# Performance work log

Measured on AMD Instinct MI355X. Metric: run time of the kernel, lower is better.

Reference implementation:

```python
import jax, jax.numpy as jnp
import numpy as np

D_MODEL = 41
D_STATE = 16
D_CONV = 4
EXPAND = 2
D_INNER = EXPAND * D_MODEL  # 82
DT_RANK = (D_MODEL + D_STATE - 1) // D_STATE  # ceil(41/16) = 3
NUM_LABELS = 10
B, L = 32, 8192


def setup_inputs() -> dict:
    key = jax.random.key(0)
    ks = jax.random.split(key, 12)
    s = 0.02
    inp = {
        "input": jax.random.normal(ks[0], (B, L, D_MODEL), dtype=jnp.float32),
        # Mamba params
        "in_proj_w": jax.random.normal(ks[1], (2 * D_INNER, D_MODEL), dtype=jnp.float32) * s,
        "conv_w": jax.random.normal(ks[2], (D_INNER, D_CONV), dtype=jnp.float32) * s,
        "conv_b": jnp.zeros((D_INNER,), dtype=jnp.float32),
        "x_proj_w": jax.random.normal(ks[3], (DT_RANK + 2 * D_STATE, D_INNER), dtype=jnp.float32) * s,
        "dt_proj_w": jax.random.normal(ks[4], (D_INNER, DT_RANK), dtype=jnp.float32) * s,
        "dt_proj_b": jax.random.normal(ks[5], (D_INNER,), dtype=jnp.float32) * s,
        "A_log": jnp.log(jnp.broadcast_to(jnp.arange(1, D_STATE + 1, dtype=jnp.float32), (D_INNER, D_STATE))),
        "D": jnp.ones((D_INNER,), dtype=jnp.float32),
        "out_proj_w": jax.random.normal(ks[6], (D_MODEL, D_INNER), dtype=jnp.float32) * s,
        # classifier
        "cls_w": jax.random.normal(ks[7], (NUM_LABELS, D_MODEL), dtype=jnp.float32) * s,
        "cls_b": jnp.zeros((NUM_LABELS,), dtype=jnp.float32),
    }
    return inp


def _mamba(x, in_proj_w, conv_w, conv_b, x_proj_w, dt_proj_w, dt_proj_b, A_log, D, out_proj_w):
    Bsz, Lseq, _ = x.shape
    # input projection -> x branch and gate z: [B, L, 2*d_inner]
    xz = jnp.einsum("bld,ed->ble", x, in_proj_w)
    xs, z = jnp.split(xz, 2, axis=-1)  # each [B, L, d_inner]

    # depthwise causal conv1d (kernel d_conv) via shifted sums
    xp = jnp.pad(xs, ((0, 0), (D_CONV - 1, 0), (0, 0)))
    xc = conv_b
    for k in range(D_CONV):
        xc = xc + xp[:, k:k + Lseq, :] * conv_w[:, k]
    xc = jax.nn.silu(xc)  # [B, L, d_inner]

    # input-dependent SSM params
    xdbc = jnp.einsum("bld,ed->ble", xc, x_proj_w)  # [B, L, dt_rank + 2*d_state]
    dt = xdbc[..., :DT_RANK]
    Bm = xdbc[..., DT_RANK:DT_RANK + D_STATE]          # [B, L, d_state]
    Cm = xdbc[..., DT_RANK + D_STATE:]                 # [B, L, d_state]
    delta = jax.nn.softplus(jnp.einsum("blr,dr->bld", dt, dt_proj_w) + dt_proj_b)  # [B, L, d_inner]

    A = -jnp.exp(A_log)  # [d_inner, d_state]

    # selective scan: h_t = exp(delta_t A) h_{t-1} + delta_t B_t x_t ; y_t = <h_t, C_t>
    dA = jnp.exp(delta[..., None] * A)                         # [B, L, d_inner, d_state]
    dBx = delta[..., None] * Bm[:, :, None, :] * xc[..., None]  # [B, L, d_inner, d_state]

    def step(h, inputs):
        dA_t, dBx_t, C_t = inputs
        h = dA_t * h + dBx_t                      # [B, d_inner, d_state]
        y_t = jnp.einsum("bds,bs->bd", h, C_t)
        return h, y_t

    h0 = jnp.zeros((Bsz, D_INNER, D_STATE), dtype=x.dtype)
    _, ys = jax.lax.scan(
        step, h0,
        (jnp.swapaxes(dA, 0, 1), jnp.swapaxes(dBx, 0, 1), jnp.swapaxes(Cm, 0, 1)))
    y = jnp.swapaxes(ys, 0, 1) + xc * D  # [B, L, d_inner]
    y = y * jax.nn.silu(z)
    return jnp.einsum("ble,de->bld", y, out_proj_w)  # [B, L, d_model]


def reference(input, in_proj_w, conv_w, conv_b, x_proj_w, dt_proj_w, dt_proj_b,
              A_log, D, out_proj_w, cls_w, cls_b):
    out = _mamba(input, in_proj_w, conv_w, conv_b, x_proj_w, dt_proj_w, dt_proj_b,
                 A_log, D, out_proj_w)
    logits = jnp.einsum("bld,nd->bln", out, cls_w) + cls_b
    return logits
```

## Files before the change

kernel.cpp:

```cpp
#include <hip/hip_runtime.h>
#include <math.h>


namespace {
constexpr int DMODEL=41, DIN=82, NSTATE=16, NLAB=10, BATCH=32, SEQ=8192;
constexpr int CHUNK=512, NCHUNK=SEQ/CHUNK, TSUB=16, NSUB=CHUNK/TSUB, RWS=TSUB+3;
constexpr int XPAD=44, SPAD=83, CPAD=84, JPAD=36;
constexpr int NPH_OLD = BATCH*NCHUNK*DIN*NSTATE;
constexpr int T0 = 64;
constexpr int FREC = 180;
inline size_t tier_bytes(int P){
  size_t SEG = (size_t)SEQ/P, tiles = SEG/T0;
  return ((size_t)BATCH*SEG*FREC + 3*((size_t)BATCH*tiles*1312)
          + (size_t)BATCH*1312 + 4096)*4;
}
}

__device__ __forceinline__ float siluf(float v)     { return v / (1.f + expf(-v)); }
__device__ __forceinline__ float softplusf(float v) { return (v > 20.f) ? v : log1pf(expf(v)); }
__device__ __forceinline__ float silu_f(float v){
  return v * __builtin_amdgcn_rcpf(1.f + __expf(-v));
}
__device__ __forceinline__ float softplus_f(float v){
  return (v > 20.f) ? v : __logf(1.f + __expf(v));
}

template<int NR>
__device__ __forceinline__ void inproj_rows(int r0, int e,
    const float* __restrict__ sx, const float* __restrict__ wt,
    float* __restrict__ sxs) {
  float acc[NR];
#pragma unroll
  for (int i=0;i<NR;i++) acc[i]=0.f;
#pragma unroll
  for (int kq=0;kq<40;kq+=4){
    const float w0=wt[(kq+0)*82+e], w1=wt[(kq+1)*82+e];
    const float w2=wt[(kq+2)*82+e], w3=wt[(kq+3)*82+e];
#pragma unroll
    for (int i=0;i<NR;i++){
      const float4 xv = *(const float4*)&sx[(r0+i)*44+kq];
      acc[i]=fmaf(xv.x,w0,acc[i]); acc[i]=fmaf(xv.y,w1,acc[i]);
      acc[i]=fmaf(xv.z,w2,acc[i]); acc[i]=fmaf(xv.w,w3,acc[i]);
    }
  }
  const float wl = wt[40*82+e];
#pragma unroll
  for (int i=0;i<NR;i++)
    sxs[(r0+i)*82+e] = fmaf(sx[(r0+i)*44+40], wl, acc[i]);
}


__global__ __launch_bounds__(256) void k_pre(
    const float* __restrict__ w_out, const float* __restrict__ w_cls,
    float* __restrict__ M){
  const int w = blockIdx.x*256 + threadIdx.x;
  if (w < NLAB*DIN){
    const int n = w/82, dd = w - n*82;
    float a = 0.f;
#pragma unroll
    for (int dm=0;dm<41;dm++) a = fmaf(w_cls[n*41+dm], w_out[dm*82+dd], a);
    M[w] = a;
  }
}

__launch_bounds__(256, 4)
__global__ void k0_feat(
    const float* __restrict__ xg, const float* __restrict__ w_in,
    const float* __restrict__ w_conv, const float* __restrict__ b_conv,
    const float* __restrict__ w_xproj, const float* __restrict__ w_dt,
    const float* __restrict__ b_dt, const float* __restrict__ A_log,
    const float* __restrict__ Dvec, int off, int SEG,
    float* __restrict__ feat, float* __restrict__ Pg, float* __restrict__ Hg)
{
  __shared__ float s_x[19*44];
  __shared__ float s_xs[19*82];
  __shared__ float s_xc[16*82];
  __shared__ float s_q[16*82];
  __shared__ float s_db[16*36];
  __shared__ float w_t[41*82];
  __shared__ float s_cw[4*82];
  __shared__ float s_dtw[3*82];
  __shared__ float s_cb[82], s_dtb[82], s_A0[82], s_Dv[82];
  __shared__ int   s_flag[82];

  const int tid = threadIdx.x;
  const int tile = blockIdx.x, b = blockIdx.y;
  const int base_pos = off + tile*T0;

  for (int i=tid;i<41*82;i+=256){ int k=i/82,e=i-k*82; w_t[i]=w_in[e*41+k]; }
  for (int i=tid;i<328;i+=256){ int dd=i/4,k=i-dd*4; s_cw[k*82+dd]=w_conv[i]; }
  for (int i=tid;i<246;i+=256){ int dd=i/3,k=i-dd*3; s_dtw[k*82+dd]=w_dt[i]; }
  if (tid<82){
    s_cb[tid]=b_conv[tid]; s_dtb[tid]=b_dt[tid]; s_Dv[tid]=Dvec[tid];
    float A0=-expf(A_log[tid*16]); s_A0[tid]=A0;
    bool ok=(A0<0.f);
#pragma unroll
    for (int s=1;s<16;s++){
      float As=-expf(A_log[tid*16+s]);
      ok = ok && (fabsf(As-(float)(s+1)*A0) <= 1e-3f*(float)(s+1)*fabsf(A0));
    }
    s_flag[tid]=ok?1:0;
  }
  __syncthreads();

  const int d = tid>>1, sg = tid&1;
  float h[8], As[8], A0d=-1.f, Dp=0.f;
  int flag=1;
  if (tid<164){
    flag = s_flag[d]; A0d = s_A0[d];
    if (!flag){
#pragma unroll
      for (int i=0;i<8;i++) As[i]=-expf(A_log[d*16+sg*8+i]);
    }
#pragma unroll
    for (int i=0;i<8;i++) h[i]=0.f;
  }

  for (int it=0; it<T0/16; ++it){
    const int p0 = base_pos + it*16;
    if (it>0){
      for (int i=tid;i<246;i+=256){ int r=i/82, dd=i-r*82; s_xs[r*82+dd]=s_xs[(16+r)*82+dd]; }
    }
    {
      const int rlo=(it==0)?0:3, cnt=(19-rlo)*41;
      for (int i=tid;i<cnt;i+=256){
        int r=rlo+i/41, k=i-(i/41)*41;
        int pos=p0-3+r;
        s_x[r*44+k] = (pos>=0) ? xg[((size_t)b*SEQ+(size_t)pos)*41+k] : 0.f;
      }
    }
    __syncthreads();
    if (tid<164){
      const int e=(tid<82)?tid:tid-82, rh=(tid>=82);
      if (it==0){ if(!rh) inproj_rows<10>(0,e,s_x,w_t,s_xs); else inproj_rows<9>(10,e,s_x,w_t,s_xs); }
      else      { inproj_rows<8>(rh?11:3,e,s_x,w_t,s_xs); }
    }
    __syncthreads();
    for (int w=tid;w<1312;w+=256){
      const int l=w&15, dd=w>>4;
      float a=s_cb[dd];
#pragma unroll
      for (int k=0;k<4;k++) a=fmaf(s_xs[(l+k)*82+dd], s_cw[k*82+dd], a);
      s_xc[l*82+dd]=silu_f(a);
    }
    __syncthreads();
    for (int w=tid;w<560;w+=256){
      const int l=w&15, j=w>>4;
      const float2* wp=(const float2*)(w_xproj + j*82);
      const float2* gp=(const float2*)&s_xc[l*82];
      float a=0.f;
#pragma unroll
      for (int dq=0;dq<41;dq++){
        const float2 wv=wp[dq], gv=gp[dq];
        a=fmaf(wv.x,gv.x,a); a=fmaf(wv.y,gv.y,a);
      }
      const int col=(j<3)?j:j+1;
      s_db[l*36+col]=a;
    }
    __syncthreads();
    for (int w=tid;w<1312;w+=256){
      const int l=w&15, dd=w>>4;
      float a=s_dtb[dd];
      a=fmaf(s_db[l*36+0],s_dtw[0*82+dd],a);
      a=fmaf(s_db[l*36+1],s_dtw[1*82+dd],a);
      a=fmaf(s_db[l*36+2],s_dtw[2*82+dd],a);
      s_q[l*82+dd]=softplus_f(a);
    }
    __syncthreads();
    if (tid<164){
#pragma unroll 1
      for (int l=0;l<16;l++){
        const float dl  = s_q[l*82+d];
        const float xc  = s_xc[l*82+d];
        const float dxc = dl*xc;
        Dp += dl;
        const float4 B0=*(const float4*)&s_db[l*36+4+sg*8];
        const float4 B1=*(const float4*)&s_db[l*36+8+sg*8];
        const float4 C0=*(const float4*)&s_db[l*36+20+sg*8];
        const float4 C1=*(const float4*)&s_db[l*36+24+sg*8];
        const float Bv[8]={B0.x,B0.y,B0.z,B0.w,B1.x,B1.y,B1.z,B1.w};
        const float Cv[8]={C0.x,C0.y,C0.z,C0.w,C1.x,C1.y,C1.z,C1.w};
        float y=0.f;
        if (flag){
          const float q=__expf(dl*A0d);
          const float q2=q*q, q4=q2*q2;
          float e = sg ? q4*q4*q : q;
#pragma unroll
          for (int s=0;s<8;s++){
            h[s]=fmaf(e,h[s],dxc*Bv[s]);
            y=fmaf(h[s],Cv[s],y);
            if(s<7) e*=q;
          }
        } else {
#pragma unroll
          for (int s=0;s<8;s++){
            const float e=__expf(dl*As[s]);
            h[s]=fmaf(e,h[s],dxc*Bv[s]);
            y=fmaf(h[s],Cv[s],y);
          }
        }
        y += __shfl_down(y,1);
        if (sg==0){
          s_xc[l*82+d] = y + xc*s_Dv[d];
          s_q [l*82+d] = Dp;
        }
      }
    }
    __syncthreads();
    {
      float* fb = feat + ((size_t)b*SEG + (size_t)(tile*T0+it*16))*FREC;
      for (int i=tid;i<720;i+=256){
        const int l=i/45, q=i-l*45;
        const int f=4*q;
        float4 v;
        if (q<20){
          v.x=s_xc[l*82+f+0]; v.y=s_xc[l*82+f+1];
          v.z=s_xc[l*82+f+2]; v.w=s_xc[l*82+f+3];
        } else if (q==20){
          v.x=s_xc[l*82+80]; v.y=s_xc[l*82+81];
          v.z=s_q[l*82+0];   v.w=s_q[l*82+1];
        } else if (q<=40){
          v.x=s_q[l*82+f-82]; v.y=s_q[l*82+f-81];
          v.z=s_q[l*82+f-80]; v.w=s_q[l*82+f-79];
        } else {
          const int c=f-164;
          v.x=s_db[l*36+20+c+0]; v.y=s_db[l*36+20+c+1];
          v.z=s_db[l*36+20+c+2]; v.w=s_db[l*36+20+c+3];
        }
        *(float4*)&fb[(size_t)l*FREC + f] = v;
      }
    }
  }

  if (tid<164){
    float Pv[8];
    if (flag){
      const float Qt=__expf(Dp*A0d);
      const float Q2=Qt*Qt, Q4=Q2*Q2, Q8=Q4*Q4;
      float c = sg ? Q8*Qt : Qt;
#pragma unroll
      for (int i=0;i<8;i++){ Pv[i]=c; c*=Qt; }
    } else {
#pragma unroll
      for (int i=0;i<8;i++) Pv[i]=__expf(Dp*As[i]);
    }
    const size_t base = ((size_t)(b*gridDim.x+tile))*1312 + (size_t)d*16 + sg*8;
    *(float4*)&Pg[base]   = make_float4(Pv[0],Pv[1],Pv[2],Pv[3]);
    *(float4*)&Pg[base+4] = make_float4(Pv[4],Pv[5],Pv[6],Pv[7]);
    *(float4*)&Hg[base]   = make_float4(h[0],h[1],h[2],h[3]);
    *(float4*)&Hg[base+4] = make_float4(h[4],h[5],h[6],h[7]);
  }
}

__global__ __launch_bounds__(256) void k2_comb(
    const float* __restrict__ Pg, const float* __restrict__ Hg,
    float* __restrict__ Hin, float* __restrict__ carry, int TPP, int first)
{
  const int g = blockIdx.x*256 + threadIdx.x;
  const int b = g/1312, r = g - b*1312;
  float h = first ? 0.f : carry[g];
#pragma unroll 4
  for (int t=0;t<TPP;t++){
    const size_t idx = ((size_t)(b*TPP+t))*1312 + r;
    Hin[idx]=h;
    h = fmaf(Pg[idx], h, Hg[idx]);
  }
  carry[g]=h;
}

__launch_bounds__(256, 4)
__global__ void k4_out(
    const float* __restrict__ xg, const float* __restrict__ w_in,
    const float* __restrict__ A_log, const float* __restrict__ Mg,
    const float* __restrict__ b_cls, int off, int SEG,
    const float* __restrict__ feat, const float* __restrict__ Hin,
    float* __restrict__ outg)
{
  __shared__ float s_x[16*44];
  __shared__ float w_zt[41*82];
  __shared__ float s_z[16*82];
  __shared__ float s_g[16*82];
  __shared__ float s_c[16*16];
  __shared__ float s_hin[1312];
  __shared__ float s_M[10*82];
  __shared__ float s_A0[82], s_bc[10];
  __shared__ int   s_flag[82];

  const int tid = threadIdx.x;
  const int tile = blockIdx.x, b = blockIdx.y;

  for (int i=tid;i<41*82;i+=256){ int k=i/82,e=i-k*82; w_zt[i]=w_in[(82+e)*41+k]; }
  for (int i=tid;i<1312;i+=256){
    const int dd=i>>4, s=i&15;
    s_hin[s*82+dd] = Hin[((size_t)(b*gridDim.x+tile))*1312 + i];
  }
  for (int i=tid;i<820;i+=256) s_M[i]=Mg[i];
  if (tid<10) s_bc[tid]=b_cls[tid];
  if (tid<82){
    float A0=-expf(A_log[tid*16]); s_A0[tid]=A0;
    bool ok=(A0<0.f);
#pragma unroll
    for (int s=1;s<16;s++){
      float As=-expf(A_log[tid*16+s]);
      ok = ok && (fabsf(As-(float)(s+1)*A0) <= 1e-3f*(float)(s+1)*fabsf(A0));
    }
    s_flag[tid]=ok?1:0;
  }
  int lk[6], dk[6];
#pragma unroll
  for (int k=0;k<6;k++){ const int w=tid+256*k; lk[k]=w/82; dk[k]=w-lk[k]*82; }

  for (int it=0; it<T0/16; ++it){
    const int lp0 = tile*T0 + it*16;
    const int gp0 = off + lp0;
    __syncthreads();
    for (int i=tid;i<656;i+=256){
      const int r=i/41, k=i-r*41;
      s_x[r*44+k] = xg[((size_t)b*SEQ+(size_t)(gp0+r))*41+k];
    }
    for (int i=tid;i<64;i+=256){
      const int l=i>>2, q=i&3;
      ((float4*)&s_c[l*16])[q] =
          ((const float4*)(feat + ((size_t)b*SEG+(size_t)(lp0+l))*FREC + 164))[q];
    }
    __syncthreads();
    if (tid<164){
      const int e=(tid<82)?tid:tid-82, l0=(tid>=82)?8:0;
      float acc[8];
#pragma unroll
      for (int i=0;i<8;i++) acc[i]=0.f;
#pragma unroll
      for (int kq=0;kq<40;kq+=4){
        const float w0=w_zt[(kq+0)*82+e], w1=w_zt[(kq+1)*82+e];
        const float w2=w_zt[(kq+2)*82+e], w3=w_zt[(kq+3)*82+e];
#pragma unroll
        for (int i=0;i<8;i++){
          const float4 xv=*(const float4*)&s_x[(l0+i)*44+kq];
          acc[i]=fmaf(xv.x,w0,acc[i]); acc[i]=fmaf(xv.y,w1,acc[i]);
          acc[i]=fmaf(xv.z,w2,acc[i]); acc[i]=fmaf(xv.w,w3,acc[i]);
        }
      }
      const float wl=w_zt[40*82+e];
#pragma unroll
      for (int i=0;i<8;i++)
        s_z[(l0+i)*82+e] = silu_f(fmaf(s_x[(l0+i)*44+40], wl, acc[i]));
    }
    __syncthreads();
#pragma unroll
    for (int k=0;k<6;k++){
      const int w=tid+256*k;
      if (w>=1312) break;
      const int l=lk[k], dd=dk[k];
      const float* fp = feat + ((size_t)b*SEG+(size_t)(lp0+l))*FREC;
      const float yl = fp[dd];
      const float Dp = fp[82+dd];
      float acc=yl;
      if (s_flag[dd]){
        const float Qt=__expf(s_A0[dd]*Dp);
        float e=Qt;
#pragma unroll
        for (int s=0;s<16;s++){
          acc = fmaf(s_c[l*16+s]*e, s_hin[s*82+dd], acc);
          if (s<15) e*=Qt;
        }
      } else {
#pragma unroll
        for (int s=0;s<16;s++){
          const float As = -__expf(A_log[dd*16+s]);
          acc = fmaf(s_c[l*16+s]*__expf(As*Dp), s_hin[s*82+dd], acc);
        }
      }
      s_g[l*82+dd] = acc * s_z[l*82+dd];
    }
    __syncthreads();
    if (tid<160){
      const int l=tid/10, n=tid-(tid/10)*10;
      float a=s_bc[n];
      const float2* gp=(const float2*)&s_g[l*82];
      const float2* mp=(const float2*)&s_M[n*82];
#pragma unroll
      for (int q=0;q<41;q++){
        const float2 gv=gp[q], mv=mp[q];
        a=fmaf(gv.x,mv.x,a); a=fmaf(gv.y,mv.y,a);
      }
      outg[((size_t)b*SEQ+(size_t)gp0)*10 + tid] = a;
    }
  }
}


template <int PASS>
__launch_bounds__(256, 2)
__global__ void mamba_chunk(
    const float* __restrict__ xg, const float* __restrict__ w_in,
    const float* __restrict__ w_conv, const float* __restrict__ b_conv,
    const float* __restrict__ w_xproj, const float* __restrict__ w_dt,
    const float* __restrict__ b_dt, const float* __restrict__ A_log,
    const float* __restrict__ Dvec, const float* __restrict__ w_out,
    const float* __restrict__ w_cls, const float* __restrict__ b_cls,
    float* __restrict__ Pg, float* __restrict__ Hg,
    const float* __restrict__ Hin, float* __restrict__ outg)
{
  __shared__ float s_x[RWS*XPAD];
  __shared__ float s_xs[RWS*SPAD];
  __shared__ float s_xc[TSUB*CPAD];
  __shared__ float s_z[TSUB*SPAD];
  __shared__ float s_xdbc[TSUB*JPAD];
  __shared__ float w_in_t[DMODEL*164];
  __shared__ float w_xp_t[DIN*35];
  __shared__ float s_cw[DIN*4];
  __shared__ float s_cb[DIN];
  __shared__ float s_dtw[DIN*3];
  __shared__ float s_dtb[DIN];

  const int tid=threadIdx.x;
  const int b=blockIdx.x/NCHUNK, c=blockIdx.x%NCHUNK, l0c=c*CHUNK;
  constexpr int NJ=(PASS==3)?35:19;
  constexpr int NE=(PASS==3)?164:DIN;

  for (int i=tid;i<DMODEL*164;i+=256){ int k=i/164,e=i-k*164; w_in_t[i]=w_in[e*DMODEL+k]; }
  for (int i=tid;i<DIN*35;i+=256){ int dd=i/35,j=i-dd*35; w_xp_t[i]=w_xproj[j*DIN+dd]; }
  for (int i=tid;i<DIN*4;i+=256) s_cw[i]=w_conv[i];
  for (int i=tid;i<DIN*3;i+=256) s_dtw[i]=w_dt[i];
  if (tid<DIN){ s_cb[tid]=b_conv[tid]; s_dtb[tid]=b_dt[tid]; }

  float h[NSTATE], Pp[NSTATE], As[NSTATE];
  float A0=-1.f, Dd=0.f;
  bool structured=true;
  if (tid<DIN){
#pragma unroll
    for (int s=0;s<NSTATE;++s) As[s]=-expf(A_log[tid*NSTATE+s]);
    A0=As[0];
#pragma unroll
    for (int s=0;s<NSTATE;++s)
      structured = structured && (fabsf(As[s]-(float)(s+1)*A0)<=1e-3f*(float)(s+1)*fabsf(A0));
    structured = structured && (A0<0.f);
    if (PASS==3){
      Dd=Dvec[tid];
      size_t base=((size_t)(b*NCHUNK+c))*(DIN*NSTATE)+(size_t)tid*NSTATE;
#pragma unroll
      for (int s=0;s<NSTATE;++s) h[s]=Hin[base+s];
    } else {
#pragma unroll
      for (int s=0;s<NSTATE;++s){ h[s]=0.f; Pp[s]=1.f; }
    }
  }
  __syncthreads();

  for (int t=0;t<NSUB;++t){
    const int p0=l0c+t*TSUB;
    for (int i=tid;i<RWS*DMODEL;i+=256){
      int r=i/DMODEL,k=i-r*DMODEL;
      int pos=p0-3+r;
      s_x[r*XPAD+k]=(pos>=0)?xg[(size_t)b*SEQ*DMODEL+(size_t)pos*DMODEL+k]:0.f;
    }
    __syncthreads();
    {
      const int e=tid;
      if (e<NE){
        float acc[RWS];
#pragma unroll
        for (int r=0;r<RWS;++r) acc[r]=0.f;
#pragma unroll
        for (int kq=0;kq<40;kq+=4){
          const float w0=w_in_t[(kq+0)*164+e], w1=w_in_t[(kq+1)*164+e];
          const float w2=w_in_t[(kq+2)*164+e], w3=w_in_t[(kq+3)*164+e];
#pragma unroll
          for (int r=0;r<RWS;++r){
            const float4 xv=*(const float4*)&s_x[r*XPAD+kq];
            acc[r]=fmaf(xv.x,w0,acc[r]); acc[r]=fmaf(xv.y,w1,acc[r]);
            acc[r]=fmaf(xv.z,w2,acc[r]); acc[r]=fmaf(xv.w,w3,acc[r]);
          }
        }
        const float wl=w_in_t[40*164+e];
#pragma unroll
        for (int r=0;r<RWS;++r) acc[r]=fmaf(s_x[r*XPAD+40],wl,acc[r]);
        if (e<DIN){
#pragma unroll
          for (int r=0;r<RWS;++r) s_xs[r*SPAD+e]=acc[r];
        } else {
#pragma unroll
          for (int r=3;r<RWS;++r) s_z[(r-3)*SPAD+(e-DIN)]=acc[r];
        }
      }
    }
    __syncthreads();
    for (int w=tid;w<TSUB*DIN;w+=256){
      const int l=w&15,e=w>>4;
      float a=s_cb[e];
#pragma unroll
      for (int k=0;k<4;++k) a=fmaf(s_xs[(l+k)*SPAD+e],s_cw[e*4+k],a);
      s_xc[l*CPAD+e]=siluf(a);
    }
    __syncthreads();
    for (int w=tid;w<TSUB*NJ;w+=256){
      const int l=w&15,j=w>>4;
      float a=0.f;
#pragma unroll
      for (int dq=0;dq<80;dq+=4){
        const float4 xv=*(const float4*)&s_xc[l*CPAD+dq];
        a=fmaf(xv.x,w_xp_t[(dq+0)*35+j],a); a=fmaf(xv.y,w_xp_t[(dq+1)*35+j],a);
        a=fmaf(xv.z,w_xp_t[(dq+2)*35+j],a); a=fmaf(xv.w,w_xp_t[(dq+3)*35+j],a);
      }
      a=fmaf(s_xc[l*CPAD+80],w_xp_t[80*35+j],a);
      a=fmaf(s_xc[l*CPAD+81],w_xp_t[81*35+j],a);
      const int col=(j<3)?j:j+1;
      s_xdbc[l*JPAD+col]=a;
    }
    __syncthreads();
    for (int w=tid;w<TSUB*DIN;w+=256){
      const int l=w&15,dd=w>>4;
      float a=s_dtb[dd];
      a=fmaf(s_xdbc[l*JPAD+0],s_dtw[dd*3+0],a);
      a=fmaf(s_xdbc[l*JPAD+1],s_dtw[dd*3+1],a);
      a=fmaf(s_xdbc[l*JPAD+2],s_dtw[dd*3+2],a);
      s_xs[l*SPAD+dd]=softplusf(a);
    }
    __syncthreads();
    if (tid<DIN){
      const int dd=tid;
#pragma unroll 1
      for (int l=0;l<TSUB;++l){
        const float dl=s_xs[l*SPAD+dd];
        const float xcd=s_xc[l*CPAD+dd];
        const float dxc=dl*xcd;
        const float4 B0=*(const float4*)&s_xdbc[l*JPAD+4];
        const float4 B1=*(const float4*)&s_xdbc[l*JPAD+8];
        const float4 B2=*(const float4*)&s_xdbc[l*JPAD+12];
        const float4 B3=*(const float4*)&s_xdbc[l*JPAD+16];
        const float Bv[NSTATE]={B0.x,B0.y,B0.z,B0.w,B1.x,B1.y,B1.z,B1.w,
                                B2.x,B2.y,B2.z,B2.w,B3.x,B3.y,B3.z,B3.w};
        float Cv[NSTATE];
        if (PASS==3){
          const float4 C0=*(const float4*)&s_xdbc[l*JPAD+20];
          const float4 C1=*(const float4*)&s_xdbc[l*JPAD+24];
          const float4 C2=*(const float4*)&s_xdbc[l*JPAD+28];
          const float4 C3=*(const float4*)&s_xdbc[l*JPAD+32];
          Cv[0]=C0.x;Cv[1]=C0.y;Cv[2]=C0.z;Cv[3]=C0.w;
          Cv[4]=C1.x;Cv[5]=C1.y;Cv[6]=C1.z;Cv[7]=C1.w;
          Cv[8]=C2.x;Cv[9]=C2.y;Cv[10]=C2.z;Cv[11]=C2.w;
          Cv[12]=C3.x;Cv[13]=C3.y;Cv[14]=C3.z;Cv[15]=C3.w;
        }
        float y=(PASS==3)?Dd*xcd:0.f;
        if (structured){
          const float q=expf(dl*A0);
          float e=q;
#pragma unroll
          for (int s=0;s<NSTATE;++s){
            h[s]=fmaf(e,h[s],dxc*Bv[s]);
            if (PASS==1) Pp[s]*=e; else y=fmaf(h[s],Cv[s],y);
            if (s<NSTATE-1) e*=q;
          }
        } else {
#pragma unroll
          for (int s=0;s<NSTATE;++s){
            const float e=expf(dl*As[s]);
            h[s]=fmaf(e,h[s],dxc*Bv[s]);
            if (PASS==1) Pp[s]*=e; else y=fmaf(h[s],Cv[s],y);
          }
        }
        if (PASS==3) s_xs[l*SPAD+dd]=y;
      }
    }
    __syncthreads();
    if (PASS==3){
      for (int w=tid;w<TSUB*DIN;w+=256){
        const int l=w&15,dd=w>>4;
        s_xc[l*CPAD+dd]=s_xs[l*SPAD+dd]*siluf(s_z[l*SPAD+dd]);
      }
      __syncthreads();
      for (int w=tid;w<TSUB*DMODEL;w+=256){
        const int l=w&15,dm=w>>4;
        const float2* wp=(const float2*)(w_out+dm*DIN);
        const float2* gp=(const float2*)&s_xc[l*CPAD];
        float a=0.f;
#pragma unroll
        for (int dq=0;dq<41;++dq){
          const float2 wv=wp[dq], gv=gp[dq];
          a=fmaf(wv.x,gv.x,a); a=fmaf(wv.y,gv.y,a);
        }
        s_x[l*XPAD+dm]=a;
      }
      __syncthreads();
      for (int w=tid;w<TSUB*NLAB;w+=256){
        const int l=w&15,n=w>>4;
        float a=b_cls[n];
#pragma unroll
        for (int dm=0;dm<DMODEL;++dm) a=fmaf(w_cls[n*DMODEL+dm],s_x[l*XPAD+dm],a);
        s_xdbc[l*NLAB+n]=a;
      }
      __syncthreads();
      for (int i=tid;i<TSUB*NLAB;i+=256)
        outg[((size_t)(b*SEQ+p0))*NLAB+i]=s_xdbc[i];
      __syncthreads();
    }
  }

  if (PASS==1 && tid<DIN){
    size_t base=((size_t)(b*NCHUNK+c))*(DIN*NSTATE)+(size_t)tid*NSTATE;
#pragma unroll
    for (int s=0;s<NSTATE;++s){ Pg[base+s]=Pp[s]; Hg[base+s]=h[s]; }
  }
}

__global__ __launch_bounds__(256) void mamba_combine(
    const float* __restrict__ P, const float* __restrict__ H, float* __restrict__ Hin){
  const int g=blockIdx.x*256+threadIdx.x;
  const int b=g/(DIN*NSTATE), ds=g-b*(DIN*NSTATE);
  float h=0.f;
#pragma unroll 1
  for (int c=0;c<NCHUNK;++c){
    const size_t idx=((size_t)(b*NCHUNK+c))*(DIN*NSTATE)+ds;
    Hin[idx]=h;
    h=fmaf(P[idx],h,H[idx]);
  }
}


extern "C" void kernel_launch(void* const* d_in, const int* in_sizes, int n_in,
                              void* d_out, int out_size, void* d_ws, size_t ws_size,
                              hipStream_t stream) {
  const float* xg     = (const float*)d_in[0];
  const float* w_in   = (const float*)d_in[1];
  const float* w_conv = (const float*)d_in[2];
  const float* b_conv = (const float*)d_in[3];
  const float* w_xp   = (const float*)d_in[4];
  const float* w_dt   = (const float*)d_in[5];
  const float* b_dt   = (const float*)d_in[6];
  const float* A_log  = (const float*)d_in[7];
  const float* Dv     = (const float*)d_in[8];
  const float* w_out  = (const float*)d_in[9];
  const float* w_cls  = (const float*)d_in[10];
  const float* b_cls  = (const float*)d_in[11];
  float* outg = (float*)d_out;

  int P = 0;
  for (int p : {1,2,4,8}) if (ws_size >= tier_bytes(p)) { P = p; break; }

  if (P) {
    const int SEG = SEQ/P, tiles = SEG/T0;
    const size_t featF = (size_t)BATCH*SEG*FREC;
    const size_t phF   = (size_t)BATCH*tiles*1312;
    float* feat  = (float*)d_ws;
    float* Pg    = feat + featF;
    float* Hg    = Pg + phF;
    float* Hin   = Hg + phF;
    float* carry = Hin + phF;
    float* Mg    = carry + (size_t)BATCH*1312;
    k_pre<<<dim3(4),256,0,stream>>>(w_out, w_cls, Mg);
    for (int p=0;p<P;p++){
      const int off = p*SEG;
      k0_feat<<<dim3(tiles,BATCH),256,0,stream>>>(
          xg,w_in,w_conv,b_conv,w_xp,w_dt,b_dt,A_log,Dv,off,SEG,feat,Pg,Hg);
      k2_comb<<<dim3((BATCH*1312)/256),256,0,stream>>>(Pg,Hg,Hin,carry,tiles,p==0?1:0);
      k4_out<<<dim3(tiles,BATCH),256,0,stream>>>(
          xg,w_in,A_log,Mg,b_cls,off,SEG,feat,Hin,outg);
    }
  } else {
    float* Pg  = (float*)d_ws;
    float* Hg  = Pg + NPH_OLD;
    float* Hin = Hg + NPH_OLD;
    dim3 grid(BATCH*NCHUNK), blk(256);
    mamba_chunk<1><<<grid,blk,0,stream>>>(xg,w_in,w_conv,b_conv,w_xp,w_dt,b_dt,
                                          A_log,Dv,w_out,w_cls,b_cls,Pg,Hg,nullptr,nullptr);
    mamba_combine<<<dim3((BATCH*DIN*NSTATE)/256),blk,0,stream>>>(Pg,Hg,Hin);
    mamba_chunk<3><<<grid,blk,0,stream>>>(xg,w_in,w_conv,b_conv,w_xp,w_dt,b_dt,
                                          A_log,Dv,w_out,w_cls,b_cls,nullptr,nullptr,Hin,outg);
  }
}
```

Before: 643.8 us.

## Keep in_proj weights in registers split across thread pairs and pad feature rows

Each thread pair now holds half of one in_proj weight row in registers and reduces with a shuffle, replacing the shared-memory transposed weight tile in both the feature and output kernels. This removes the per-block weight staging and frees a large amount of LDS, which may raise occupancy. Shared arrays and the feature record are padded to 84/184 floats so reads and writes can use aligned float4 accesses. The non-geometric A path now recomputes exp(A_log) inline instead of caching it, and the in-projection loses its multi-row register blocking, so it does more LDS reads of x per FMA.

Measured after the change: 703.9 us. 9.3% more time.

```diff
diff --git a/kernel.cpp b/kernel.cpp
--- a/kernel.cpp
+++ b/kernel.cpp
@@ -8,7 +8,7 @@
 constexpr int XPAD=44, SPAD=83, CPAD=84, JPAD=36;
 constexpr int NPH_OLD = BATCH*NCHUNK*DIN*NSTATE;
 constexpr int T0 = 64;
-constexpr int FREC = 180;
+constexpr int FREC = 184;
 inline size_t tier_bytes(int P){
   size_t SEG = (size_t)SEQ/P, tiles = SEG/T0;
   return ((size_t)BATCH*SEG*FREC + 3*((size_t)BATCH*tiles*1312)
@@ -23,30 +23,6 @@
 }
 __device__ __forceinline__ float softplus_f(float v){
   return (v > 20.f) ? v : __logf(1.f + __expf(v));
-}
-
-template<int NR>
-__device__ __forceinline__ void inproj_rows(int r0, int e,
-    const float* __restrict__ sx, const float* __restrict__ wt,
-    float* __restrict__ sxs) {
-  float acc[NR];
-#pragma unroll
-  for (int i=0;i<NR;i++) acc[i]=0.f;
-#pragma unroll
-  for (int kq=0;kq<40;kq+=4){
-    const float w0=wt[(kq+0)*82+e], w1=wt[(kq+1)*82+e];
-    const float w2=wt[(kq+2)*82+e], w3=wt[(kq+3)*82+e];
-#pragma unroll
-    for (int i=0;i<NR;i++){
-      const float4 xv = *(const float4*)&sx[(r0+i)*44+kq];
-      acc[i]=fmaf(xv.x,w0,acc[i]); acc[i]=fmaf(xv.y,w1,acc[i]);
-      acc[i]=fmaf(xv.z,w2,acc[i]); acc[i]=fmaf(xv.w,w3,acc[i]);
-    }
-  }
-  const float wl = wt[40*82+e];
-#pragma unroll
-  for (int i=0;i<NR;i++)
-    sxs[(r0+i)*82+e] = fmaf(sx[(r0+i)*44+40], wl, acc[i]);
 }
 
 
@@ -74,10 +50,9 @@
 {
   __shared__ float s_x[19*44];
   __shared__ float s_xs[19*82];
-  __shared__ float s_xc[16*82];
-  __shared__ float s_q[16*82];
+  __shared__ float s_xc[16*84];
+  __shared__ float s_q[16*84];
   __shared__ float s_db[16*36];
-  __shared__ float w_t[41*82];
   __shared__ float s_cw[4*82];
   __shared__ float s_dtw[3*82];
   __shared__ float s_cb[82], s_dtb[82], s_A0[82], s_Dv[82];
@@ -87,7 +62,6 @@
   const int tile = blockIdx.x, b = blockIdx.y;
   const int base_pos = off + tile*T0;
 
-  for (int i=tid;i<41*82;i+=256){ int k=i/82,e=i-k*82; w_t[i]=w_in[e*41+k]; }
   for (int i=tid;i<328;i+=256){ int dd=i/4,k=i-dd*4; s_cw[k*82+dd]=w_conv[i]; }
   for (int i=tid;i<246;i+=256){ int dd=i/3,k=i-dd*3; s_dtw[k*82+dd]=w_dt[i]; }
   if (tid<82){
@@ -101,17 +75,24 @@
     }
     s_flag[tid]=ok?1:0;
   }
+
+  const int d = tid>>1, sg = tid&1;
+  float wreg[21];
+#pragma unroll
+  for (int t=0;t<21;t++) wreg[t]=0.f;
+  if (tid<164){
+#pragma unroll
+    for (int t=0;t<21;t++){
+      if (sg)          wreg[t]=w_in[d*41+20+t];
+      else if (t<20)   wreg[t]=w_in[d*41+t];
+    }
+  }
   __syncthreads();
 
-  const int d = tid>>1, sg = tid&1;
-  float h[8], As[8], A0d=-1.f, Dp=0.f;
+  float h[8], A0d=-1.f, Dp=0.f;
   int flag=1;
   if (tid<164){
     flag = s_flag[d]; A0d = s_A0[d];
-    if (!flag){
-#pragma unroll
-      for (int i=0;i<8;i++) As[i]=-expf(A_log[d*16+sg*8+i]);
-    }
 #pragma unroll
     for (int i=0;i<8;i++) h[i]=0.f;
   }
@@ -131,9 +112,22 @@
     }
     __syncthreads();
     if (tid<164){
-      const int e=(tid<82)?tid:tid-82, rh=(tid>=82);
-      if (it==0){ if(!rh) inproj_rows<10>(0,e,s_x,w_t,s_xs); else inproj_rows<9>(10,e,s_x,w_t,s_xs); }
-      else      { inproj_rows<8>(rh?11:3,e,s_x,w_t,s_xs); }
+      const int kb = sg*20;
+      auto bodyB = [&](int r){
+        float a=0.f;
+#pragma unroll
+        for (int q=0;q<5;q++){
+          const float4 xv = *(const float4*)&s_x[r*44+kb+4*q];
+          a=fmaf(xv.x,wreg[4*q+0],a); a=fmaf(xv.y,wreg[4*q+1],a);
+          a=fmaf(xv.z,wreg[4*q+2],a); a=fmaf(xv.w,wreg[4*q+3],a);
+        }
+        if (sg) a=fmaf(s_x[r*44+40], wreg[20], a);
+        const float tot = a + __shfl_down(a,1);
+        if (!sg) s_xs[r*82+d]=tot;
+      };
+      if (it==0){ bodyB(0); bodyB(1); bodyB(2); }
+#pragma unroll 4
+      for (int r=3;r<19;++r) bodyB(r);
     }
     __syncthreads();
     for (int w=tid;w<1312;w+=256){
@@ -141,18 +135,24 @@
       float a=s_cb[dd];
 #pragma unroll
       for (int k=0;k<4;k++) a=fmaf(s_xs[(l+k)*82+dd], s_cw[k*82+dd], a);
-      s_xc[l*82+dd]=silu_f(a);
+      s_xc[l*84+dd]=silu_f(a);
     }
     __syncthreads();
     for (int w=tid;w<560;w+=256){
       const int l=w&15, j=w>>4;
       const float2* wp=(const float2*)(w_xproj + j*82);
-      const float2* gp=(const float2*)&s_xc[l*82];
+      const float4* gp=(const float4*)&s_xc[l*84];
       float a=0.f;
 #pragma unroll
-      for (int dq=0;dq<41;dq++){
-        const float2 wv=wp[dq], gv=gp[dq];
-        a=fmaf(wv.x,gv.x,a); a=fmaf(wv.y,gv.y,a);
+      for (int dq=0;dq<20;dq++){
+        const float4 gv=gp[dq];
+        const float2 w0=wp[2*dq], w1=wp[2*dq+1];
+        a=fmaf(gv.x,w0.x,a); a=fmaf(gv.y,w0.y,a);
+        a=fmaf(gv.z,w1.x,a); a=fmaf(gv.w,w1.y,a);
+      }
+      {
+        const float2 w0=wp[40];
+        a=fmaf(s_xc[l*84+80],w0.x,a); a=fmaf(s_xc[l*84+81],w0.y,a);
       }
       const int col=(j<3)?j:j+1;
       s_db[l*36+col]=a;
@@ -164,14 +164,14 @@
       a=fmaf(s_db[l*36+0],s_dtw[0*82+dd],a);
       a=fmaf(s_db[l*36+1],s_dtw[1*82+dd],a);
       a=fmaf(s_db[l*36+2],s_dtw[2*82+dd],a);
-      s_q[l*82+dd]=softplus_f(a);
+      s_q[l*84+dd]=softplus_f(a);
     }
     __syncthreads();
     if (tid<164){
 #pragma unroll 1
       for (int l=0;l<16;l++){
-        const float dl  = s_q[l*82+d];
-        const float xc  = s_xc[l*82+d];
+        const float dl  = s_q[l*84+d];
+        const float xc  = s_xc[l*84+d];
         const float dxc = dl*xc;
         Dp += dl;
         const float4 B0=*(const float4*)&s_db[l*36+4+sg*8];
@@ -194,40 +194,36 @@
         } else {
 #pragma unroll
           for (int s=0;s<8;s++){
-            const float e=__expf(dl*As[s]);
+            const float e=__expf(dl*(-__expf(A_log[d*16+sg*8+s])));
             h[s]=fmaf(e,h[s],dxc*Bv[s]);
             y=fmaf(h[s],Cv[s],y);
           }
         }
         y += __shfl_down(y,1);
         if (sg==0){
-          s_xc[l*82+d] = y + xc*s_Dv[d];
-          s_q [l*82+d] = Dp;
+          s_xc[l*84+d] = y + xc*s_Dv[d];
+          s_q [l*84+d] = Dp;
         }
       }
     }
     __syncthreads();
     {
       float* fb = feat + ((size_t)b*SEG + (size_t)(tile*T0+it*16))*FREC;
-      for (int i=tid;i<720;i+=256){
-        const int l=i/45, q=i-l*45;
-        const int f=4*q;
+      for (int i=tid;i<736;i+=256){
+        const int l=i/46, q=i-l*46;
         float4 v;
         if (q<20){
-          v.x=s_xc[l*82+f+0]; v.y=s_xc[l*82+f+1];
-          v.z=s_xc[l*82+f+2]; v.w=s_xc[l*82+f+3];
+          v = *(const float4*)&s_xc[l*84+4*q];
         } else if (q==20){
-          v.x=s_xc[l*82+80]; v.y=s_xc[l*82+81];
-          v.z=s_q[l*82+0];   v.w=s_q[l*82+1];
-        } else if (q<=40){
-          v.x=s_q[l*82+f-82]; v.y=s_q[l*82+f-81];
-          v.z=s_q[l*82+f-80]; v.w=s_q[l*82+f-79];
+          v.x=s_xc[l*84+80]; v.y=s_xc[l*84+81]; v.z=0.f; v.w=0.f;
+        } else if (q<41){
+          v = *(const float4*)&s_q[l*84+4*(q-21)];
+        } else if (q==41){
+          v.x=s_q[l*84+80]; v.y=s_q[l*84+81]; v.z=0.f; v.w=0.f;
         } else {
-          const int c=f-164;
-          v.x=s_db[l*36+20+c+0]; v.y=s_db[l*36+20+c+1];
-          v.z=s_db[l*36+20+c+2]; v.w=s_db[l*36+20+c+3];
-        }
-        *(float4*)&fb[(size_t)l*FREC + f] = v;
+          v = *(const float4*)&s_db[l*36+20+4*(q-42)];
+        }
+        *(float4*)&fb[(size_t)l*FREC + 4*q] = v;
       }
     }
   }
@@ -242,7 +238,7 @@
       for (int i=0;i<8;i++){ Pv[i]=c; c*=Qt; }
     } else {
 #pragma unroll
-      for (int i=0;i<8;i++) Pv[i]=__expf(Dp*As[i]);
+      for (int i=0;i<8;i++) Pv[i]=__expf(Dp*(-__expf(A_log[d*16+sg*8+i])));
     }
     const size_t base = ((size_t)(b*gridDim.x+tile))*1312 + (size_t)d*16 + sg*8;
     *(float4*)&Pg[base]   = make_float4(Pv[0],Pv[1],Pv[2],Pv[3]);
@@ -277,7 +273,6 @@
     float* __restrict__ outg)
 {
   __shared__ float s_x[16*44];
-  __shared__ float w_zt[41*82];
   __shared__ float s_z[16*82];
   __shared__ float s_g[16*82];
   __shared__ float s_c[16*16];
@@ -289,7 +284,6 @@
   const int tid = threadIdx.x;
   const int tile = blockIdx.x, b = blockIdx.y;
 
-  for (int i=tid;i<41*82;i+=256){ int k=i/82,e=i-k*82; w_zt[i]=w_in[(82+e)*41+k]; }
   for (int i=tid;i<1312;i+=256){
     const int dd=i>>4, s=i&15;
     s_hin[s*82+dd] = Hin[((size_t)(b*gridDim.x+tile))*1312 + i];
@@ -306,6 +300,17 @@
     }
     s_flag[tid]=ok?1:0;
   }
+  const int ez = tid>>1, sgz = tid&1;
+  float wz[21];
+#pragma unroll
+  for (int t=0;t<21;t++) wz[t]=0.f;
+  if (tid<164){
+#pragma unroll
+    for (int t=0;t<21;t++){
+      if (sgz)        wz[t]=w_in[(82+ez)*41+20+t];
+      else if (t<20)  wz[t]=w_in[(82+ez)*41+t];
+    }
+  }
   int lk[6], dk[6];
 #pragma unroll
   for (int k=0;k<6;k++){ const int w=tid+256*k; lk[k]=w/82; dk[k]=w-lk[k]*82; }
@@ -321,29 +326,24 @@
     for (int i=tid;i<64;i+=256){
       const int l=i>>2, q=i&3;
       ((float4*)&s_c[l*16])[q] =
-          ((const float4*)(feat + ((size_t)b*SEG+(size_t)(lp0+l))*FREC + 164))[q];
+          ((const float4*)(feat + ((size_t)b*SEG+(size_t)(lp0+l))*FREC + 168))[q];
     }
     __syncthreads();
     if (tid<164){
-      const int e=(tid<82)?tid:tid-82, l0=(tid>=82)?8:0;
-      float acc[8];
-#pragma unroll
-      for (int i=0;i<8;i++) acc[i]=0.f;
-#pragma unroll
-      for (int kq=0;kq<40;kq+=4){
-        const float w0=w_zt[(kq+0)*82+e], w1=w_zt[(kq+1)*82+e];
-        const float w2=w_zt[(kq+2)*82+e], w3=w_zt[(kq+3)*82+e];
-#pragma unroll
-        for (int i=0;i<8;i++){
-          const float4 xv=*(const float4*)&s_x[(l0+i)*44+kq];
-          acc[i]=fmaf(xv.x,w0,acc[i]); acc[i]=fmaf(xv.y,w1,acc[i]);
-          acc[i]=fmaf(xv.z,w2,acc[i]); acc[i]=fmaf(xv.w,w3,acc[i]);
-        }
-      }
-      const float wl=w_zt[40*82+e];
-#pragma unroll
-      for (int i=0;i<8;i++)
-        s_z[(l0+i)*82+e] = silu_f(fmaf(s_x[(l0+i)*44+40], wl, acc[i]));
+      const int kb = sgz*20;
+#pragma unroll 4
+      for (int r=0;r<16;++r){
+        float a=0.f;
+#pragma unroll
+        for (int q=0;q<5;q++){
+          const float4 xv=*(const float4*)&s_x[r*44+kb+4*q];
+          a=fmaf(xv.x,wz[4*q+0],a); a=fmaf(xv.y,wz[4*q+1],a);
+          a=fmaf(xv.z,wz[4*q+2],a); a=fmaf(xv.w,wz[4*q+3],a);
+        }
+        if (sgz) a=fmaf(s_x[r*44+40], wz[20], a);
+        const float tot = a + __shfl_down(a,1);
+        if (!sgz) s_z[r*82+ez] = silu_f(tot);
+      }
     }
     __syncthreads();
 #pragma unroll
@@ -353,7 +353,7 @@
       const int l=lk[k], dd=dk[k];
       const float* fp = feat + ((size_t)b*SEG+(size_t)(lp0+l))*FREC;
       const float yl = fp[dd];
-      const float Dp = fp[82+dd];
+      const float Dp = fp[84+dd];
       float acc=yl;
       if (s_flag[dd]){
         const float Qt=__expf(s_A0[dd]*Dp);
```
